# Performance work log

Measured on AMD Instinct MI355X. Metric: run time of the kernel, lower is better.

Reference implementation:

```python
import jax, jax.numpy as jnp
import numpy as np

CH = 64
CF = CH // 8  # f/g projection channels


def setup_inputs() -> dict:
    key = jax.random.key(0)
    k1, k2, k3, k4, k5 = jax.random.split(key, 5)
    x = jax.random.normal(k1, (8, 64, 64, CH), dtype=jnp.float32)
    kernel_f = 0.02 * jax.random.normal(k2, (1, 1, CH, CF), dtype=jnp.float32)
    kernel_g = 0.02 * jax.random.normal(k3, (1, 1, CH, CF), dtype=jnp.float32)
    kernel_h = 0.02 * jax.random.normal(k4, (1, 1, CH, CH), dtype=jnp.float32)
    gamma = 0.02 * jax.random.normal(k5, (1,), dtype=jnp.float32)
    return {"x": x, "kernel_f": kernel_f, "kernel_g": kernel_g,
            "kernel_h": kernel_h, "gamma": gamma}


def reference(x, kernel_f, kernel_g, kernel_h, gamma):
    B, H, W, C = x.shape
    N = H * W
    xf = x.reshape(B, N, C)  # flatten spatial; 1x1 conv == matmul over channels
    f = jnp.einsum('bnc,cd->bnd', xf, kernel_f[0, 0])  # [B,N,CF]
    g = jnp.einsum('bnc,cd->bnd', xf, kernel_g[0, 0])  # [B,N,CF]
    h = jnp.einsum('bnc,cd->bnd', xf, kernel_h[0, 0])  # [B,N,C]
    s = jnp.einsum('bnd,bmd->bnm', g, f)  # g @ f^T, [B,N,N]
    beta = jax.nn.softmax(s, axis=-1)
    o = jnp.einsum('bnm,bmc->bnc', beta, h)  # [B,N,C]
    out = gamma * o.reshape(B, H, W, C) + x
    return out
```

## Files before the change

kernel.cpp:

```cpp
#include <hip/hip_runtime.h>
#include <hip/hip_bf16.h>

typedef __attribute__((ext_vector_type(4)))  float f32x4;
typedef __attribute__((ext_vector_type(16))) float f32x16;
typedef __attribute__((ext_vector_type(8)))  short bf16x8;

#define LOG2E 1.44269504088896340736f

#if __has_builtin(__builtin_amdgcn_exp2f)
static __device__ __forceinline__ float exp2_native(float x) {
  return __builtin_amdgcn_exp2f(x);
}
#else
extern "C" __device__ float __ocml_native_exp2_f32(float);
static __device__ __forceinline__ float exp2_native(float x) {
  return __ocml_native_exp2_f32(x);
}
#endif

static __device__ __forceinline__ unsigned int pack_trunc_f(float a, float b) {
  return __builtin_amdgcn_perm(__float_as_uint(b), __float_as_uint(a), 0x07060302);
}

typedef const __attribute__((address_space(1))) unsigned int gu32;
typedef __attribute__((address_space(3))) unsigned int lu32;
static __device__ __forceinline__ void gload_lds16(const void* g, void* l) {
  __builtin_amdgcn_global_load_lds((gu32*)g, (lu32*)l, 16, 0, 0);
}

__global__ __launch_bounds__(256) void proj_kernel(
    const float* __restrict__ x, const float* __restrict__ kf,
    const float* __restrict__ kg, const float* __restrict__ kh,
    unsigned short* __restrict__ f_b, unsigned short* __restrict__ g_b,
    unsigned short* __restrict__ h_p)
{
  __shared__ unsigned short Kt[80*72];
  const int t = threadIdx.x, blk = blockIdx.x;

  #pragma unroll
  for (int r = 0; r < 20; ++r) {
    int idx = r*256 + t;
    int o = idx >> 6, c = idx & 63;
    float v = (o < 8) ? kf[c*8 + o]
            : (o < 16) ? kg[c*8 + (o-8)] * LOG2E
            : kh[c*64 + (o-16)];
    Kt[o*72 + c] = (unsigned short)(__float_as_uint(v) >> 16);
  }
  __syncthreads();

  const int w = t >> 6, lane = t & 63, l15 = lane & 15, quad = lane >> 4;
  const int Rbase = blk*64 + w*16;
  const int R = Rbase + l15;

  bf16x8 af[2];
  #pragma unroll
  for (int kk = 0; kk < 2; ++kk) {
    const float* xp = x + (long)R*64 + kk*32 + quad*8;
    float4 v0 = *(const float4*)xp;
    float4 v1 = *(const float4*)(xp + 4);
    union { unsigned int u[4]; bf16x8 v; } p;
    p.u[0] = pack_trunc_f(v0.x, v0.y);
    p.u[1] = pack_trunc_f(v0.z, v0.w);
    p.u[2] = pack_trunc_f(v1.x, v1.y);
    p.u[3] = pack_trunc_f(v1.z, v1.w);
    af[kk] = p.v;
  }

  f32x4 acc[5];
  #pragma unroll
  for (int nt = 0; nt < 5; ++nt) { f32x4 z = {}; acc[nt] = z; }

  #pragma unroll
  for (int nt = 0; nt < 5; ++nt)
    #pragma unroll
    for (int kk = 0; kk < 2; ++kk) {
      bf16x8 bfv = *(const bf16x8*)&Kt[(nt*16 + l15)*72 + kk*32 + quad*8];
      acc[nt] = __builtin_amdgcn_mfma_f32_16x16x32_bf16(af[kk], bfv, acc[nt], 0, 0, 0);
    }

  const int bt = Rbase >> 12;
  const int kt = (Rbase >> 7) & 31;
  const int base = ((blk & 1) << 6) + (w << 4);
  const int pi = base + ((quad & 1) << 3) + (((quad >> 1) & 1) << 2);

  #pragma unroll
  for (int rr = 0; rr < 4; ++rr) {
    const int nq = (Rbase + quad*4 + rr) & 4095;
    unsigned short v = (unsigned short)(__float_as_uint(acc[0][rr]) >> 16);
    if (l15 < 8) f_b[((long)bt*4096 + nq)*8 + l15] = v;
    else         g_b[((long)bt*4096 + nq)*8 + (l15 - 8)] = v;
  }
  #pragma unroll
  for (int nt = 1; nt < 5; ++nt) {
    const int c = (nt - 1)*16 + l15;
    uint2 v;
    v.x = pack_trunc_f(acc[nt][0], acc[nt][1]);
    v.y = pack_trunc_f(acc[nt][2], acc[nt][3]);
    *(uint2*)(h_p + ((long)(bt*32 + kt)*64 + c)*136 + pi) = v;
  }
}

__global__ __launch_bounds__(128, 4) void attn_kernel(
    const unsigned short* __restrict__ f_b, const unsigned short* __restrict__ g_b,
    const unsigned short* __restrict__ h_p, unsigned short* __restrict__ po,
    float* __restrict__ pl)
{
  __shared__ unsigned short hts[64*136];
  __shared__ unsigned short fts[128*8];

  const int t = threadIdx.x;
  const int w = t >> 6, lane = t & 63, l31 = lane & 31, a = lane >> 5;
  const int qb = blockIdx.x, b = blockIdx.y, sp = blockIdx.z;
  const int q0w = qb*64 + w*32;

  bf16x8 gf;
  {
    bf16x8 gv = *(const bf16x8*)(g_b + ((long)b*4096 + q0w + l31)*8);
    bf16x8 z = {};
    gf = (a == 0) ? gv : z;
  }

  f32x16 oacc[2];
  { f32x16 z = {}; oacc[0] = z; oacc[1] = z; }
  float l_run = 0.f;

  const char* hp_b = (const char*)h_p + (long)b*32*17408;
  const char* fb_b = (const char*)f_b + (long)b*4096*16;

  for (int ktl = 0; ktl < 8; ++ktl) {
    const int kt = sp*8 + ktl;
    __syncthreads();
    const char* hsrc = hp_b + (long)kt*17408;
    const char* fsrc = fb_b + (long)kt*2048;
    if (w == 0) {
      #pragma unroll
      for (int i = 0; i < 9; ++i)
        gload_lds16(hsrc + i*1024 + lane*16, (char*)hts + i*1024);
      gload_lds16(fsrc + lane*16, (char*)fts);
    } else {
      #pragma unroll
      for (int i = 9; i < 17; ++i)
        gload_lds16(hsrc + i*1024 + lane*16, (char*)hts + i*1024);
      gload_lds16(fsrc + 1024 + lane*16, (char*)fts + 1024);
    }
    __syncthreads();

    #pragma unroll
    for (int mt = 0; mt < 4; ++mt) {
      bf16x8 afv = *(const bf16x8*)&fts[(mt*32 + l31)*8];
      f32x16 zz = {};
      f32x16 sc = __builtin_amdgcn_mfma_f32_32x32x16_bf16(afv, gf, zz, 0, 0, 0);

      float e[16];
      #pragma unroll
      for (int r = 0; r < 16; ++r) {
        e[r] = exp2_native(sc[r]);
        l_run += e[r];
      }

      #pragma unroll
      for (int half = 0; half < 2; ++half) {
        const int s = mt*2 + half;
        union { unsigned int u[4]; bf16x8 v; } ap;
        ap.u[0] = pack_trunc_f(e[half*8+0], e[half*8+1]);
        ap.u[1] = pack_trunc_f(e[half*8+2], e[half*8+3]);
        ap.u[2] = pack_trunc_f(e[half*8+4], e[half*8+5]);
        ap.u[3] = pack_trunc_f(e[half*8+6], e[half*8+7]);
        #pragma unroll
        for (int nt = 0; nt < 2; ++nt) {
          bf16x8 bh = *(const bf16x8*)&hts[(nt*32 + l31)*136 + s*16 + a*8];
          oacc[nt] = __builtin_amdgcn_mfma_f32_32x32x16_bf16(ap.v, bh, oacc[nt], 0, 0, 0);
        }
      }
    }
  }

  l_run += __shfl_xor(l_run, 32);
  const long sb = (long)sp*8 + b;
  if (lane < 32) pl[(sb << 12) + q0w + l31] = l_run;

  unsigned short* pob = po + ((sb << 12) + q0w)*64;
  #pragma unroll
  for (int nt = 0; nt < 2; ++nt)
    #pragma unroll
    for (int r = 0; r < 16; ++r) {
      const int q = (r & 3) + 8*(r >> 2) + 4*a;
      pob[(long)q*64 + nt*32 + l31] =
          (unsigned short)(__float_as_uint(oacc[nt][r]) >> 16);
    }
}

__global__ __launch_bounds__(256) void combine_kernel(
    const float* __restrict__ x, const unsigned short* __restrict__ po,
    const float* __restrict__ pl, const float* __restrict__ gamma_p,
    float* __restrict__ out)
{
  const long tid = (long)blockIdx.x*256 + threadIdx.x;
  const long bn = tid >> 3;
  const int c0 = (int)(tid & 7)*8;

  float l = 0.f;
  float o[8];
  #pragma unroll
  for (int i = 0; i < 8; ++i) o[i] = 0.f;
  #pragma unroll
  for (int s = 0; s < 4; ++s) {
    l += pl[(long)s*32768 + bn];
    uint4 v = *(const uint4*)(po + ((long)s*32768 + bn)*64 + c0);
    const unsigned short* pv = (const unsigned short*)&v;
    #pragma unroll
    for (int i = 0; i < 8; ++i)
      o[i] += __uint_as_float((unsigned int)pv[i] << 16);
  }
  const float scale = gamma_p[0] / l;
  const float* xp = x + bn*64 + c0;
  float4 x0 = *(const float4*)xp;
  float4 x1 = *(const float4*)(xp + 4);
  float4 r0, r1;
  r0.x = fmaf(scale, o[0], x0.x);
  r0.y = fmaf(scale, o[1], x0.y);
  r0.z = fmaf(scale, o[2], x0.z);
  r0.w = fmaf(scale, o[3], x0.w);
  r1.x = fmaf(scale, o[4], x1.x);
  r1.y = fmaf(scale, o[5], x1.y);
  r1.z = fmaf(scale, o[6], x1.z);
  r1.w = fmaf(scale, o[7], x1.w);
  float* op = out + bn*64 + c0;
  *(float4*)op = r0;
  *(float4*)(op + 4) = r1;
}

extern "C" void kernel_launch(void* const* d_in, const int* in_sizes, int n_in,
                              void* d_out, int out_size, void* d_ws, size_t ws_size,
                              hipStream_t stream) {
  const float* x  = (const float*)d_in[0];
  const float* kf = (const float*)d_in[1];
  const float* kg = (const float*)d_in[2];
  const float* kh = (const float*)d_in[3];
  const float* gamma = (const float*)d_in[4];
  float* out = (float*)d_out;

  char* ws = (char*)d_ws;
  unsigned short* h_p = (unsigned short*)ws;
  unsigned short* f_b = (unsigned short*)(ws + 4456448);
  unsigned short* g_b = (unsigned short*)(ws + 4980736);
  unsigned short* po  = (unsigned short*)(ws + 5505024);
  float*          pl  = (float*)(ws + 22282240);

  proj_kernel<<<512, 256, 0, stream>>>(x, kf, kg, kh, f_b, g_b, h_p);
  attn_kernel<<<dim3(64, 8, 4), 128, 0, stream>>>(f_b, g_b, h_p, po, pl);
  combine_kernel<<<1024, 256, 0, stream>>>(x, po, pl, gamma, out);
}
```

Before: 104.5 us.

## Double-buffer K/V tiles and process two query groups per wave in attention

Each wave now handles 64 queries (two 32-query groups), so every LDS-loaded h/f tile is reused across twice as many MFMAs, and the block count halves. The LDS staging becomes double-buffered: the next key tile's global-to-LDS load is issued before computing on the current one, removing one barrier per iteration. Register pressure doubles (four 32x32 accumulators), so launch bounds drop occupancy to 2, and the grid has fewer blocks, which risks less latency hiding.

```diff
diff --git a/kernel.cpp b/kernel.cpp
--- a/kernel.cpp
+++ b/kernel.cpp
@@ -100,94 +100,107 @@
   }
 }
 
-__global__ __launch_bounds__(128, 4) void attn_kernel(
+__global__ __launch_bounds__(128, 2) void attn_kernel(
     const unsigned short* __restrict__ f_b, const unsigned short* __restrict__ g_b,
     const unsigned short* __restrict__ h_p, unsigned short* __restrict__ po,
     float* __restrict__ pl)
 {
-  __shared__ unsigned short hts[64*136];
-  __shared__ unsigned short fts[128*8];
+  __shared__ unsigned short bufs[2][9728];
 
   const int t = threadIdx.x;
   const int w = t >> 6, lane = t & 63, l31 = lane & 31, a = lane >> 5;
   const int qb = blockIdx.x, b = blockIdx.y, sp = blockIdx.z;
-  const int q0w = qb*64 + w*32;
-
-  bf16x8 gf;
-  {
-    bf16x8 gv = *(const bf16x8*)(g_b + ((long)b*4096 + q0w + l31)*8);
+  const int q0w = qb*128 + w*64;
+
+  bf16x8 gf[2];
+  #pragma unroll
+  for (int qg = 0; qg < 2; ++qg) {
+    bf16x8 gv = *(const bf16x8*)(g_b + ((long)b*4096 + q0w + qg*32 + l31)*8);
     bf16x8 z = {};
-    gf = (a == 0) ? gv : z;
-  }
-
-  f32x16 oacc[2];
-  { f32x16 z = {}; oacc[0] = z; oacc[1] = z; }
-  float l_run = 0.f;
+    gf[qg] = (a == 0) ? gv : z;
+  }
+
+  f32x16 oacc[2][2];
+  { f32x16 z = {}; oacc[0][0] = z; oacc[0][1] = z; oacc[1][0] = z; oacc[1][1] = z; }
+  float l_run[2] = {0.f, 0.f};
 
   const char* hp_b = (const char*)h_p + (long)b*32*17408;
   const char* fb_b = (const char*)f_b + (long)b*4096*16;
 
-  for (int ktl = 0; ktl < 8; ++ktl) {
-    const int kt = sp*8 + ktl;
-    __syncthreads();
+  auto stage = [&](int bi, int kt) {
     const char* hsrc = hp_b + (long)kt*17408;
     const char* fsrc = fb_b + (long)kt*2048;
+    char* dst = (char*)&bufs[bi][0];
+    #pragma unroll
+    for (int i = 0; i < 8; ++i)
+      gload_lds16(hsrc + i*2048 + w*1024 + lane*16, dst + i*2048 + w*1024);
     if (w == 0) {
-      #pragma unroll
-      for (int i = 0; i < 9; ++i)
-        gload_lds16(hsrc + i*1024 + lane*16, (char*)hts + i*1024);
-      gload_lds16(fsrc + lane*16, (char*)fts);
+      gload_lds16(hsrc + 16384 + lane*16, dst + 16384);
     } else {
-      #pragma unroll
-      for (int i = 9; i < 17; ++i)
-        gload_lds16(hsrc + i*1024 + lane*16, (char*)hts + i*1024);
-      gload_lds16(fsrc + 1024 + lane*16, (char*)fts + 1024);
+      gload_lds16(fsrc + lane*16,        dst + 17408);
+      gload_lds16(fsrc + 1024 + lane*16, dst + 17408 + 1024);
     }
+  };
+
+  stage(0, sp*8);
+
+  for (int ktl = 0; ktl < 8; ++ktl) {
     __syncthreads();
+    if (ktl < 7) stage((ktl + 1) & 1, sp*8 + ktl + 1);
+
+    const unsigned short* hts = &bufs[ktl & 1][0];
+    const unsigned short* fts = &bufs[ktl & 1][8704];
 
     #pragma unroll
     for (int mt = 0; mt < 4; ++mt) {
       bf16x8 afv = *(const bf16x8*)&fts[(mt*32 + l31)*8];
       f32x16 zz = {};
-      f32x16 sc = __builtin_amdgcn_mfma_f32_32x32x16_bf16(afv, gf, zz, 0, 0, 0);
-
-      float e[16];
+      f32x16 sc0 = __builtin_amdgcn_mfma_f32_32x32x16_bf16(afv, gf[0], zz, 0, 0, 0);
+      f32x16 sc1 = __builtin_amdgcn_mfma_f32_32x32x16_bf16(afv, gf[1], zz, 0, 0, 0);
+
+      float e0[16], e1[16];
       #pragma unroll
       for (int r = 0; r < 16; ++r) {
-        e[r] = exp2_native(sc[r]);
-        l_run += e[r];
+        e0[r] = exp2_native(sc0[r]);
+        e1[r] = exp2_native(sc1[r]);
+        l_run[0] += e0[r];
+        l_run[1] += e1[r];
       }
 
       #pragma unroll
       for (int half = 0; half < 2; ++half) {
         const int s = mt*2 + half;
-        union { unsigned int u[4]; bf16x8 v; } ap;
-        ap.u[0] = pack_trunc_f(e[half*8+0], e[half*8+1]);
-        ap.u[1] = pack_trunc_f(e[half*8+2], e[half*8+3]);
-        ap.u[2] = pack_trunc_f(e[half*8+4], e[half*8+5]);
-        ap.u[3] = pack_trunc_f(e[half*8+6], e[half*8+7]);
+        bf16x8 bh0 = *(const bf16x8*)&hts[(l31)*136      + s*16 + a*8];
+        bf16x8 bh1 = *(const bf16x8*)&hts[(32 + l31)*136 + s*16 + a*8];
+        union { unsigned int u[4]; bf16x8 v; } ap0, ap1;
         #pragma unroll
-        for (int nt = 0; nt < 2; ++nt) {
-          bf16x8 bh = *(const bf16x8*)&hts[(nt*32 + l31)*136 + s*16 + a*8];
-          oacc[nt] = __builtin_amdgcn_mfma_f32_32x32x16_bf16(ap.v, bh, oacc[nt], 0, 0, 0);
+        for (int j = 0; j < 4; ++j) {
+          ap0.u[j] = pack_trunc_f(e0[half*8 + 2*j], e0[half*8 + 2*j + 1]);
+          ap1.u[j] = pack_trunc_f(e1[half*8 + 2*j], e1[half*8 + 2*j + 1]);
         }
+        oacc[0][0] = __builtin_amdgcn_mfma_f32_32x32x16_bf16(ap0.v, bh0, oacc[0][0], 0, 0, 0);
+        oacc[0][1] = __builtin_amdgcn_mfma_f32_32x32x16_bf16(ap0.v, bh1, oacc[0][1], 0, 0, 0);
+        oacc[1][0] = __builtin_amdgcn_mfma_f32_32x32x16_bf16(ap1.v, bh0, oacc[1][0], 0, 0, 0);
+        oacc[1][1] = __builtin_amdgcn_mfma_f32_32x32x16_bf16(ap1.v, bh1, oacc[1][1], 0, 0, 0);
       }
     }
   }
 
-  l_run += __shfl_xor(l_run, 32);
   const long sb = (long)sp*8 + b;
-  if (lane < 32) pl[(sb << 12) + q0w + l31] = l_run;
-
-  unsigned short* pob = po + ((sb << 12) + q0w)*64;
-  #pragma unroll
-  for (int nt = 0; nt < 2; ++nt)
-    #pragma unroll
-    for (int r = 0; r < 16; ++r) {
-      const int q = (r & 3) + 8*(r >> 2) + 4*a;
-      pob[(long)q*64 + nt*32 + l31] =
-          (unsigned short)(__float_as_uint(oacc[nt][r]) >> 16);
-    }
+  #pragma unroll
+  for (int qg = 0; qg < 2; ++qg) {
+    float l = l_run[qg] + __shfl_xor(l_run[qg], 32);
+    if (lane < 32) pl[(sb << 12) + q0w + qg*32 + l31] = l;
+    unsigned short* pob = po + ((sb << 12) + q0w + qg*32)*64;
+    #pragma unroll
+    for (int nt = 0; nt < 2; ++nt)
+      #pragma unroll
+      for (int r = 0; r < 16; ++r) {
+        const int q = (r & 3) + 8*(r >> 2) + 4*a;
+        pob[(long)q*64 + nt*32 + l31] =
+            (unsigned short)(__float_as_uint(oacc[qg][nt][r]) >> 16);
+      }
+  }
 }
 
 __global__ __launch_bounds__(256) void combine_kernel(
@@ -248,6 +261,6 @@
   float*          pl  = (float*)(ws + 22282240);
 
   proj_kernel<<<512, 256, 0, stream>>>(x, kf, kg, kh, f_b, g_b, h_p);
-  attn_kernel<<<dim3(64, 8, 4), 128, 0, stream>>>(f_b, g_b, h_p, po, pl);
+  attn_kernel<<<dim3(32, 8, 4), 128, 0, stream>>>(f_b, g_b, h_p, po, pl);
   combine_kernel<<<1024, 256, 0, stream>>>(x, po, pl, gamma, out);
 }
```

Measured after the change: 102.7 us. Within noise of the previous version (-1.7%).

## Double-buffer attention K/V tiles in LDS and widen blocks to four waves

Applied to the files above, without the earlier changes.

The attention kernel now uses 256-thread blocks covering 128 queries, halving the grid. Each block keeps two LDS buffers and prefetches the next key tile with async global-to-LDS loads while computing on the current one, which removes the load-then-wait stall of each iteration. Tile staging is split across four waves. The exp/pack loop is restructured to pack bf16 pairs inline with split partial sums. The cost is a larger LDS footprint (about 38 KB per block) and fewer, larger blocks, which may lower occupancy or leave CUs less evenly loaded.

```diff
diff --git a/kernel.cpp b/kernel.cpp
--- a/kernel.cpp
+++ b/kernel.cpp
@@ -100,18 +100,17 @@
   }
 }
 
-__global__ __launch_bounds__(128, 4) void attn_kernel(
+__global__ __launch_bounds__(256, 4) void attn_kernel(
     const unsigned short* __restrict__ f_b, const unsigned short* __restrict__ g_b,
     const unsigned short* __restrict__ h_p, unsigned short* __restrict__ po,
     float* __restrict__ pl)
 {
-  __shared__ unsigned short hts[64*136];
-  __shared__ unsigned short fts[128*8];
+  __shared__ char bufs[2][19456];
 
   const int t = threadIdx.x;
   const int w = t >> 6, lane = t & 63, l31 = lane & 31, a = lane >> 5;
   const int qb = blockIdx.x, b = blockIdx.y, sp = blockIdx.z;
-  const int q0w = qb*64 + w*32;
+  const int q0w = qb*128 + w*32;
 
   bf16x8 gf;
   {
@@ -125,25 +124,29 @@
   float l_run = 0.f;
 
   const char* hp_b = (const char*)h_p + (long)b*32*17408;
-  const char* fb_b = (const char*)f_b + (long)b*4096*16;
-
-  for (int ktl = 0; ktl < 8; ++ktl) {
-    const int kt = sp*8 + ktl;
-    __syncthreads();
+  const char* fb_b = (const char*)f_b + (long)b*65536;
+
+  auto stage = [&](int bi, int kt) {
     const char* hsrc = hp_b + (long)kt*17408;
     const char* fsrc = fb_b + (long)kt*2048;
-    if (w == 0) {
-      #pragma unroll
-      for (int i = 0; i < 9; ++i)
-        gload_lds16(hsrc + i*1024 + lane*16, (char*)hts + i*1024);
-      gload_lds16(fsrc + lane*16, (char*)fts);
-    } else {
-      #pragma unroll
-      for (int i = 9; i < 17; ++i)
-        gload_lds16(hsrc + i*1024 + lane*16, (char*)hts + i*1024);
-      gload_lds16(fsrc + 1024 + lane*16, (char*)fts + 1024);
-    }
+    char* dst = &bufs[bi][0];
+    #pragma unroll
+    for (int i = 0; i < 4; ++i) {
+      const int r = 4*i + w;
+      gload_lds16(hsrc + r*1024 + lane*16, dst + r*1024);
+    }
+    if (w == 0)      gload_lds16(hsrc + 16*1024 + lane*16, dst + 16*1024);
+    else if (w < 3)  gload_lds16(fsrc + (w-1)*1024 + lane*16, dst + (16+w)*1024);
+  };
+
+  stage(0, sp*8);
+
+  for (int ktl = 0; ktl < 8; ++ktl) {
     __syncthreads();
+    if (ktl < 7) stage((ktl + 1) & 1, sp*8 + ktl + 1);
+
+    const unsigned short* hts = (const unsigned short*)&bufs[ktl & 1][0];
+    const unsigned short* fts = (const unsigned short*)&bufs[ktl & 1][17408];
 
     #pragma unroll
     for (int mt = 0; mt < 4; ++mt) {
@@ -151,26 +154,25 @@
       f32x16 zz = {};
       f32x16 sc = __builtin_amdgcn_mfma_f32_32x32x16_bf16(afv, gf, zz, 0, 0, 0);
 
-      float e[16];
+      unsigned int ap[2][4];
+      float la = 0.f, lb = 0.f;
       #pragma unroll
-      for (int r = 0; r < 16; ++r) {
-        e[r] = exp2_native(sc[r]);
-        l_run += e[r];
+      for (int r = 0; r < 16; r += 2) {
+        sc[r]   = exp2_native(sc[r]);
+        sc[r+1] = exp2_native(sc[r+1]);
+        la += sc[r]; lb += sc[r+1];
+        ap[r >> 3][(r & 7) >> 1] = pack_trunc_f(sc[r], sc[r+1]);
       }
+      l_run += la + lb;
 
       #pragma unroll
       for (int half = 0; half < 2; ++half) {
         const int s = mt*2 + half;
-        union { unsigned int u[4]; bf16x8 v; } ap;
-        ap.u[0] = pack_trunc_f(e[half*8+0], e[half*8+1]);
-        ap.u[1] = pack_trunc_f(e[half*8+2], e[half*8+3]);
-        ap.u[2] = pack_trunc_f(e[half*8+4], e[half*8+5]);
-        ap.u[3] = pack_trunc_f(e[half*8+6], e[half*8+7]);
-        #pragma unroll
-        for (int nt = 0; nt < 2; ++nt) {
-          bf16x8 bh = *(const bf16x8*)&hts[(nt*32 + l31)*136 + s*16 + a*8];
-          oacc[nt] = __builtin_amdgcn_mfma_f32_32x32x16_bf16(ap.v, bh, oacc[nt], 0, 0, 0);
-        }
+        bf16x8 bh0 = *(const bf16x8*)&hts[(l31)*136      + s*16 + a*8];
+        bf16x8 bh1 = *(const bf16x8*)&hts[(32 + l31)*136 + s*16 + a*8];
+        bf16x8 av = *(const bf16x8*)&ap[half][0];
+        oacc[0] = __builtin_amdgcn_mfma_f32_32x32x16_bf16(av, bh0, oacc[0], 0, 0, 0);
+        oacc[1] = __builtin_amdgcn_mfma_f32_32x32x16_bf16(av, bh1, oacc[1], 0, 0, 0);
       }
     }
   }
@@ -248,6 +250,6 @@
   float*          pl  = (float*)(ws + 22282240);
 
   proj_kernel<<<512, 256, 0, stream>>>(x, kf, kg, kh, f_b, g_b, h_p);
-  attn_kernel<<<dim3(64, 8, 4), 128, 0, stream>>>(f_b, g_b, h_p, po, pl);
+  attn_kernel<<<dim3(32, 8, 4), 256, 0, stream>>>(f_b, g_b, h_p, po, pl);
   combine_kernel<<<1024, 256, 0, stream>>>(x, po, pl, gamma, out);
 }
```

Result: no change. 103.8 us (-0.7%).
